# Optimization experiments

Hardware: AMD Instinct MI355X
Metric: run time of the kernel (lower is better)

## Reference

```python
import jax, jax.numpy as jnp
import numpy as np

D, P = 50, 2          # feature dim and max polynomial order (module defaults)
N = 32768             # batch size

def _indexset(d, p):
    # faithful numpy port of indexset(): all multi-indices of total order exactly p
    if d == 1:
        return np.full((1, 1), p, dtype=np.int64)
    blocks = []
    for i in range(p + 1):
        sub = _indexset(d - 1, p - i)
        blocks.append(np.concatenate([np.full((sub.shape[0], 1), i, np.int64), sub], axis=1))
    return np.concatenate(blocks, axis=0)

def _normal_basis(p):
    # faithful numpy port of NormalBasis(): (physicists') Hermite recurrence coefficients
    B = np.zeros((p + 1, p + 1), np.float32)
    B[0, 0] = 1.0
    if p >= 1:
        B[1, 1] = 2.0
    for i in range(1, p):
        B[i + 1, 1:i + 2] = 2.0 * B[i, :i + 1]
        B[i + 1, :i] -= 2.0 * i * B[i - 1, :i]
    return B

def setup_inputs() -> dict:
    key = jax.random.key(0)
    k1, k2 = jax.random.split(key)
    x = jax.random.normal(k1, (N, D), dtype=jnp.float32)
    mean = jax.random.normal(k2, (D,), dtype=jnp.float32)
    var = jnp.ones((D,), dtype=jnp.float32)  # divisor; ones keeps values well-scaled
    oneDbasis = jnp.asarray(_normal_basis(P))                                   # (P+1, P+1)
    idxset = jnp.asarray(np.concatenate([_indexset(D, i) for i in range(P + 1)], axis=0))  # (1326, 50)
    return {"x": x, "mean": mean, "var": var, "oneDbasis": oneDbasis, "idxset": idxset}

def reference(x, mean, var, oneDbasis, idxset):
    p1 = oneDbasis.shape[0]  # p + 1
    # per-dim normalization (original mutates x in place; same math)
    xn = (x - mean) / var                                        # (n, d)
    # PolyVal: powers 0..p then weighted sum over basis coefficients
    x_pows = xn[..., None] ** jnp.arange(p1, dtype=xn.dtype)     # (n, d, p+1)
    polyval = jnp.einsum('ndi,pi->ndp', x_pows, oneDbasis)       # (n, d, p+1)
    n = x.shape[0]
    nbasis = idxset.shape[0]
    # Phi *= polyval[:, j, idxset[:, j]] accumulated over the d feature dims
    def body(Phi, xs):
        pv_j, idx_j = xs                 # pv_j: (n, p+1), idx_j: (nbasis,)
        return Phi * pv_j[:, idx_j], None
    Phi, _ = jax.lax.scan(body,
                          jnp.ones((n, nbasis), dtype=x.dtype),
                          (jnp.transpose(polyval, (1, 0, 2)), idxset.T))
    return Phi
```

## Files before the change

### kernel.cpp

```cpp
#include <hip/hip_runtime.h>
#include <math.h>


#define DD     50
#define NBASIS 1326
#define NPAIR  (NBASIS / 2)
#define BN     16
#define BLOCK  256
#define RS     104
#define ONEOFF 52
#define H2OFF  54

__device__ __forceinline__ int col_desc(int c) {
    if (c == 0) return ONEOFF | (ONEOFF << 8);
    if (c <= DD) return (c - 1) | (ONEOFF << 8);
    int t = c - (DD + 1);
    int q = (int)((sqrtf((float)(8 * t + 1)) - 1.0f) * 0.5f);
    while ((q + 1) * (q + 2) / 2 <= t) ++q;
    while (q * (q + 1) / 2 > t) --q;
    int s = t - q * (q + 1) / 2;
    if (s == q) return (H2OFF + q) | (ONEOFF << 8);
    return s | (q << 8);
}

__global__ __launch_bounds__(BLOCK) void pce_kernel(
    const float* __restrict__ x, const float* __restrict__ mean,
    const float* __restrict__ var, const float* __restrict__ basis,
    float* __restrict__ out, int n)
{
    __shared__ float T[BN][RS];
    const int tid  = threadIdx.x;
    const int row0 = blockIdx.x * BN;

    float b10 = basis[3], b11 = basis[4], b12 = basis[5];
    float b20 = basis[6], b21 = basis[7], b22 = basis[8];

    const int p0 = tid, p1 = tid + BLOCK, p2 = tid + 2 * BLOCK;
    const bool has2 = (p2 < NPAIR);
    int2 dA = make_int2(col_desc(2 * p0), col_desc(2 * p0 + 1));
    int2 dB = make_int2(col_desc(2 * p1), col_desc(2 * p1 + 1));
    int2 dC = has2 ? make_int2(col_desc(2 * p2), col_desc(2 * p2 + 1))
                   : make_int2(ONEOFF, ONEOFF);

    for (int i = tid; i < BN * DD; i += BLOCK) {
        int r = i / DD, c = i - r * DD;
        float xv = (x[(size_t)(row0 + r) * DD + c] - mean[c]) / var[c];
        float x2 = xv * xv;
        int k = (DD - 1) - c;
        T[r][k]         = b10 + b11 * xv + b12 * x2;
        T[r][H2OFF + k] = b20 + b21 * xv + b22 * x2;
    }
    if (tid < BN) T[tid][ONEOFF] = 1.0f;
    __syncthreads();

    #pragma unroll
    for (int r = 0; r < BN; ++r) {
        const float* pvr = T[r];
        float2* orow = (float2*)(out + (size_t)(row0 + r) * NBASIS);
        float2 v;
        v.x = pvr[dA.x & 0xff] * pvr[dA.x >> 8];
        v.y = pvr[dA.y & 0xff] * pvr[dA.y >> 8];
        orow[p0] = v;
        v.x = pvr[dB.x & 0xff] * pvr[dB.x >> 8];
        v.y = pvr[dB.y & 0xff] * pvr[dB.y >> 8];
        orow[p1] = v;
        if (has2) {
            v.x = pvr[dC.x & 0xff] * pvr[dC.x >> 8];
            v.y = pvr[dC.y & 0xff] * pvr[dC.y >> 8];
            orow[p2] = v;
        }
    }
}

extern "C" void kernel_launch(void* const* d_in, const int* in_sizes, int n_in,
                              void* d_out, int out_size, void* d_ws, size_t ws_size,
                              hipStream_t stream) {
    const float* x     = (const float*)d_in[0];
    const float* mean  = (const float*)d_in[1];
    const float* var   = (const float*)d_in[2];
    const float* basis = (const float*)d_in[3];
    float* out = (float*)d_out;

    const int d = in_sizes[1];
    const int n = in_sizes[0] / d;

    (void)d_ws; (void)ws_size;

    pce_kernel<<<(n + BN - 1) / BN, BLOCK, 0, stream>>>(x, mean, var, basis, out, n);
}
```

Baseline: 184.1 us.

## Write output tile as flat float4 stream using shared-memory descriptor table

Treats each block's 16-row output tile as one contiguous buffer and writes it with float4 stores instead of per-row float2 stores. Column descriptors for a two-row period (1326 columns is odd, so rows pair up to align to float4) are precomputed into shared memory and read as int4. The shared table is also padded (k + k/8) so that gather reads hit fewer bank conflicts. This adds about 10 KB of shared memory per block and an extra descriptor load per store, which can lower occupancy.

```diff
diff --git a/kernel.cpp b/kernel.cpp
--- a/kernel.cpp
+++ b/kernel.cpp
@@ -4,23 +4,28 @@
 
 #define DD     50
 #define NBASIS 1326
-#define NPAIR  (NBASIS / 2)
 #define BN     16
 #define BLOCK  256
-#define RS     104
-#define ONEOFF 52
-#define H2OFF  54
+#define RS     120
+#define ONE    56
+#define H2OFF  64
+#define NDESC  2652
+#define GF4    5304
+#define FULLS  20
+#define TAIL   184
+
+__device__ __forceinline__ int padk(int k) { return k + (k >> 3); }
 
 __device__ __forceinline__ int col_desc(int c) {
-    if (c == 0) return ONEOFF | (ONEOFF << 8);
-    if (c <= DD) return (c - 1) | (ONEOFF << 8);
+    if (c == 0) return ONE | (ONE << 8);
+    if (c <= DD) return padk(c - 1) | (ONE << 8);
     int t = c - (DD + 1);
     int q = (int)((sqrtf((float)(8 * t + 1)) - 1.0f) * 0.5f);
     while ((q + 1) * (q + 2) / 2 <= t) ++q;
     while (q * (q + 1) / 2 > t) --q;
     int s = t - q * (q + 1) / 2;
-    if (s == q) return (H2OFF + q) | (ONEOFF << 8);
-    return s | (q << 8);
+    if (s == q) return (H2OFF + padk(q)) | (ONE << 8);
+    return padk(s) | (padk(q) << 8);
 }
 
 __global__ __launch_bounds__(BLOCK) void pce_kernel(
@@ -28,47 +33,55 @@
     const float* __restrict__ var, const float* __restrict__ basis,
     float* __restrict__ out, int n)
 {
-    __shared__ float T[BN][RS];
+    __shared__ float T[BN * RS];
+    __shared__ int   Dsc[NDESC];
     const int tid  = threadIdx.x;
     const int row0 = blockIdx.x * BN;
 
     float b10 = basis[3], b11 = basis[4], b12 = basis[5];
     float b20 = basis[6], b21 = basis[7], b22 = basis[8];
 
-    const int p0 = tid, p1 = tid + BLOCK, p2 = tid + 2 * BLOCK;
-    const bool has2 = (p2 < NPAIR);
-    int2 dA = make_int2(col_desc(2 * p0), col_desc(2 * p0 + 1));
-    int2 dB = make_int2(col_desc(2 * p1), col_desc(2 * p1 + 1));
-    int2 dC = has2 ? make_int2(col_desc(2 * p2), col_desc(2 * p2 + 1))
-                   : make_int2(ONEOFF, ONEOFF);
+    for (int e = tid; e < NDESC; e += BLOCK) {
+        int rf  = (e >= NBASIS) ? 1 : 0;
+        int col = e - rf * NBASIS;
+        Dsc[e] = col_desc(col) + rf * (RS | (RS << 8));
+    }
 
     for (int i = tid; i < BN * DD; i += BLOCK) {
         int r = i / DD, c = i - r * DD;
         float xv = (x[(size_t)(row0 + r) * DD + c] - mean[c]) / var[c];
         float x2 = xv * xv;
-        int k = (DD - 1) - c;
-        T[r][k]         = b10 + b11 * xv + b12 * x2;
-        T[r][H2OFF + k] = b20 + b21 * xv + b22 * x2;
+        int k  = (DD - 1) - c;
+        int pk = padk(k);
+        T[r * RS + pk]         = b10 + b11 * xv + b12 * x2;
+        T[r * RS + H2OFF + pk] = b20 + b21 * xv + b22 * x2;
     }
-    if (tid < BN) T[tid][ONEOFF] = 1.0f;
+    if (tid < BN) T[tid * RS + ONE] = 1.0f;
     __syncthreads();
 
+    float4* ob = (float4*)(out + (size_t)blockIdx.x * (BN * NBASIS));
+    int rm = tid;
+    int pb = 0;
     #pragma unroll
-    for (int r = 0; r < BN; ++r) {
-        const float* pvr = T[r];
-        float2* orow = (float2*)(out + (size_t)(row0 + r) * NBASIS);
-        float2 v;
-        v.x = pvr[dA.x & 0xff] * pvr[dA.x >> 8];
-        v.y = pvr[dA.y & 0xff] * pvr[dA.y >> 8];
-        orow[p0] = v;
-        v.x = pvr[dB.x & 0xff] * pvr[dB.x >> 8];
-        v.y = pvr[dB.y & 0xff] * pvr[dB.y >> 8];
-        orow[p1] = v;
-        if (has2) {
-            v.x = pvr[dC.x & 0xff] * pvr[dC.x >> 8];
-            v.y = pvr[dC.y & 0xff] * pvr[dC.y >> 8];
-            orow[p2] = v;
-        }
+    for (int s = 0; s < FULLS; ++s) {
+        const int4 d4 = *(const int4*)&Dsc[4 * rm];
+        float4 w;
+        w.x = T[(d4.x & 0xff) + pb] * T[((d4.x >> 8) & 0xff) + pb];
+        w.y = T[(d4.y & 0xff) + pb] * T[((d4.y >> 8) & 0xff) + pb];
+        w.z = T[(d4.z & 0xff) + pb] * T[((d4.z >> 8) & 0xff) + pb];
+        w.w = T[(d4.w & 0xff) + pb] * T[((d4.w >> 8) & 0xff) + pb];
+        ob[tid + BLOCK * s] = w;
+        rm += BLOCK;
+        if (rm >= 663) { rm -= 663; pb += 2 * RS; }
+    }
+    if (tid < TAIL) {
+        const int4 d4 = *(const int4*)&Dsc[4 * rm];
+        float4 w;
+        w.x = T[(d4.x & 0xff) + pb] * T[((d4.x >> 8) & 0xff) + pb];
+        w.y = T[(d4.y & 0xff) + pb] * T[((d4.y >> 8) & 0xff) + pb];
+        w.z = T[(d4.z & 0xff) + pb] * T[((d4.z >> 8) & 0xff) + pb];
+        w.w = T[(d4.w & 0xff) + pb] * T[((d4.w >> 8) & 0xff) + pb];
+        ob[tid + BLOCK * FULLS] = w;
     }
 }
 
```

Result: no change. 185.5 us (+0.7%).
